# Optimization experiments

Hardware: AMD Instinct MI355X
Metric: run time of the kernel (lower is better)

## Reference

```python
import jax, jax.numpy as jnp
import numpy as np

N, E, F_IN, F_E, HID, HEADS = 20000, 320000, 256, 32, 128, 4
NEG_SLOPE = 0.2  # PyG GATConv default negative_slope


def _segment_softmax(logits, seg, num_segments):
    # logits: [E, H] softmax over edges sharing the same destination node
    m = jax.ops.segment_max(logits, seg, num_segments=num_segments)
    m = jnp.where(jnp.isfinite(m), m, 0.0)
    e = jnp.exp(logits - m[seg])
    s = jax.ops.segment_sum(e, seg, num_segments=num_segments)
    return e / s[seg]


def _gat_layer(x, edge_attr, src, dst, W, We, a_src, a_dst, a_edge, bias, num_nodes):
    H, C = a_src.shape
    h = (x @ W).reshape(-1, H, C)            # [N, H, C]
    he = (edge_attr @ We).reshape(-1, H, C)  # [E, H, C]
    alpha = (h * a_src).sum(-1)[src] + (h * a_dst).sum(-1)[dst] + (he * a_edge).sum(-1)
    alpha = jax.nn.leaky_relu(alpha, NEG_SLOPE)          # [E, H]
    alpha = _segment_softmax(alpha, dst, num_nodes)
    out = jax.ops.segment_sum(h[src] * alpha[..., None], dst, num_segments=num_nodes)
    return out.reshape(num_nodes, H * C) + bias


def setup_inputs() -> dict:
    key = jax.random.key(0)
    ks = jax.random.split(key, 20)
    s1 = 1.0 / np.sqrt(F_IN)
    s2 = 1.0 / np.sqrt(HID * HEADS)
    se = 1.0 / np.sqrt(F_E)
    sh = 1.0 / np.sqrt(HID)
    return {
        "x": jax.random.normal(ks[0], (N, F_IN), jnp.float32),
        "edge_index": jax.random.randint(ks[1], (2, E), 0, N),
        "edge_attr": jax.random.normal(ks[2], (E, F_E), jnp.float32),
        # GAT layer 1: in=F_IN, heads=HEADS, out=HID, concat=True
        "W1": jax.random.normal(ks[3], (F_IN, HEADS * HID), jnp.float32) * s1,
        "We1": jax.random.normal(ks[4], (F_E, HEADS * HID), jnp.float32) * se,
        "as1": jax.random.normal(ks[5], (HEADS, HID), jnp.float32) * sh,
        "ad1": jax.random.normal(ks[6], (HEADS, HID), jnp.float32) * sh,
        "ae1": jax.random.normal(ks[7], (HEADS, HID), jnp.float32) * sh,
        "b1": jnp.zeros((HEADS * HID,), jnp.float32),
        # GAT layer 2: in=HEADS*HID, heads=1, out=HID
        "W2": jax.random.normal(ks[8], (HEADS * HID, HID), jnp.float32) * s2,
        "We2": jax.random.normal(ks[9], (F_E, HID), jnp.float32) * se,
        "as2": jax.random.normal(ks[10], (1, HID), jnp.float32) * sh,
        "ad2": jax.random.normal(ks[11], (1, HID), jnp.float32) * sh,
        "ae2": jax.random.normal(ks[12], (1, HID), jnp.float32) * sh,
        "b2": jnp.zeros((HID,), jnp.float32),
        # projection head: Linear(HID,HID) -> PReLU -> Linear(HID,HID)
        "P1": jax.random.normal(ks[13], (HID, HID), jnp.float32) * sh,
        "pb1": jnp.zeros((HID,), jnp.float32),
        "prelu_a": jnp.float32(0.25),
        "P2": jax.random.normal(ks[14], (HID, HID), jnp.float32) * sh,
        "pb2": jnp.zeros((HID,), jnp.float32),
    }


def reference(x, edge_index, edge_attr, W1, We1, as1, ad1, ae1, b1,
              W2, We2, as2, ad2, ae2, b2, P1, pb1, prelu_a, P2, pb2):
    # eval mode: edge dropout / feature dropout are no-ops
    ei = jnp.concatenate([edge_index, edge_index[::-1]], axis=1)  # add reversed edges
    ea = jnp.concatenate([edge_attr, edge_attr], axis=0)
    src, dst = ei[0], ei[1]
    n = x.shape[0]
    h = jax.nn.elu(_gat_layer(x, ea, src, dst, W1, We1, as1, ad1, ae1, b1, n))
    h = jax.nn.elu(_gat_layer(h, ea, src, dst, W2, We2, as2, ad2, ae2, b2, n))
    z = h @ P1 + pb1
    z = jnp.where(z > 0, z, prelu_a * z)  # PReLU (single shared parameter)
    h_proj = z @ P2 + pb2
    g = jax.nn.sigmoid(h_proj.mean(axis=0))
    return h_proj, g
```

## Files before the change

### kernel.cpp

```cpp
#include <hip/hip_runtime.h>
#include <hip/hip_bf16.h>


#define NN    20000
#define EE    320000
#define E2    640000
#define FIN   256
#define FE    32
#define HIDD  128
#define NHEAD 4
#define HH    512
#define CAP   160
#define AW    132

typedef unsigned short ushort_t;
typedef short frag8 __attribute__((ext_vector_type(8)));
typedef float f32x4 __attribute__((ext_vector_type(4)));

__device__ inline ushort_t f2bf(float f){
  unsigned x = __float_as_uint(f);
  unsigned r = (x + 0x7fffu + ((x>>16)&1u)) >> 16;
  return (ushort_t)r;
}
__device__ inline float bf2f(ushort_t u){ return __uint_as_float(((unsigned)u)<<16); }
__device__ inline float lo_of(unsigned v){ return __uint_as_float(v<<16); }
__device__ inline float hi_of(unsigned v){ return __uint_as_float(v & 0xffff0000u); }

__global__ void prep(const int* __restrict__ ei, int* __restrict__ cnt,
                     const float* __restrict__ x, ushort_t* __restrict__ xb,
                     const float* __restrict__ W1, ushort_t* __restrict__ W1t,
                     const float* __restrict__ W2, ushort_t* __restrict__ W2t,
                     const float* __restrict__ P1, ushort_t* __restrict__ P1th, ushort_t* __restrict__ P1tl,
                     const float* __restrict__ P2, ushort_t* __restrict__ P2th, ushort_t* __restrict__ P2tl,
                     const float* __restrict__ We1, const float* __restrict__ ae1,
                     const float* __restrict__ We2, const float* __restrict__ ae2,
                     float* __restrict__ v1, float* __restrict__ v2){
  int b = blockIdx.x, tid = threadIdx.x;
  if(b < 2500){
    int e = b*256 + tid;
    int dst = (e < EE) ? ei[EE + e] : ei[e - EE];
    atomicAdd(&cnt[dst], 1);
  } else if(b < 7500){
    int i = (b-2500)*256 + tid;
    float4 v = ((const float4*)x)[i];
    ushort4 o; o.x=f2bf(v.x); o.y=f2bf(v.y); o.z=f2bf(v.z); o.w=f2bf(v.w);
    ((ushort4*)xb)[i] = o;
  } else if(b < 8012){
    int idx = (b-7500)*256 + tid;
    int k = idx>>9, n = idx&511;
    W1t[n*FIN + k] = f2bf(W1[idx]);
  } else if(b < 8268){
    int idx = (b-8012)*256 + tid;
    int k = idx>>7, n = idx&127;
    W2t[n*HH + k] = f2bf(W2[idx]);
  } else if(b < 8332){
    int idx = (b-8268)*256 + tid;
    int k = idx>>7, n = idx&127;
    float v = P1[idx];
    ushort_t h = f2bf(v);
    P1th[n*HIDD + k] = h;
    P1tl[n*HIDD + k] = f2bf(v - bf2f(h));
  } else if(b < 8396){
    int idx = (b-8332)*256 + tid;
    int k = idx>>7, n = idx&127;
    float v = P2[idx];
    ushort_t h = f2bf(v);
    P2th[n*HIDD + k] = h;
    P2tl[n*HIDD + k] = f2bf(v - bf2f(h));
  } else {
    if(tid < FE*NHEAD){
      int f = tid>>2, h = tid&3;
      float s = 0.f;
      for(int c=0;c<HIDD;c++) s += We1[f*HH + h*HIDD + c] * ae1[h*HIDD + c];
      v1[f*4+h] = s;
    } else if(tid < FE*NHEAD + FE){
      int f = tid - FE*NHEAD;
      float s = 0.f;
      for(int c=0;c<HIDD;c++) s += We2[f*HIDD + c] * ae2[c];
      v2[f] = s;
    }
  }
}

__global__ void scan_k(const int* __restrict__ cnt, int* __restrict__ rowptr){
  __shared__ int sums[1024];
  int tid = threadIdx.x;
  const int per = 20;
  int base = tid*per;
  int v[20];
  if(base + per <= NN){
    #pragma unroll
    for(int q=0;q<5;q++) *(int4*)&v[q*4] = *(const int4*)&cnt[base + q*4];
  } else {
    for(int i=0;i<per;i++) v[i] = (base+i<NN)? cnt[base+i] : 0;
  }
  int s = 0;
  #pragma unroll
  for(int i=0;i<per;i++) s += v[i];
  sums[tid] = s; __syncthreads();
  for(int off=1; off<1024; off<<=1){
    int t = (tid>=off)? sums[tid-off] : 0;
    __syncthreads();
    sums[tid] += t;
    __syncthreads();
  }
  int run = (tid==0)? 0 : sums[tid-1];
  int rp[20];
  #pragma unroll
  for(int i=0;i<per;i++){ rp[i] = run; run += v[i]; }
  if(base + per <= NN){
    #pragma unroll
    for(int q=0;q<5;q++) *(int4*)&rowptr[base + q*4] = *(const int4*)&rp[q*4];
  } else {
    for(int i=0;i<per;i++) if(base+i<=NN) rowptr[base+i] = rp[i];
  }
  if(tid == 1000) rowptr[NN] = rp[0];
}

__global__ __launch_bounds__(256) void csr_gemm1(
    const int* __restrict__ ei, const float* __restrict__ ea,
    const float* __restrict__ v1, const float* __restrict__ v2,
    const int* __restrict__ rowptr, int* __restrict__ fcnt,
    int* __restrict__ csrc, float* __restrict__ cae1, float* __restrict__ cae2,
    const ushort_t* __restrict__ A, const ushort_t* __restrict__ Bt,
    ushort_t* __restrict__ C, int M,
    const float* __restrict__ as1, const float* __restrict__ ad1,
    float* __restrict__ s1n, float* __restrict__ d1n){
  __shared__ ushort_t As[128*32];
  __shared__ ushort_t Bs[128*32];
  __shared__ float sred[2][128], dred[2][128];
  __shared__ float sv1[FE*NHEAD];
  __shared__ float sv2[FE];
  int tid = threadIdx.x;
  int b = blockIdx.x;
  if(b < 1250){
    if(tid < FE*NHEAD) sv1[tid] = v1[tid];
    if(tid < FE)       sv2[tid] = v2[tid];
    __syncthreads();
    int e = b*256 + tid;
    int a = ei[e], bb = ei[EE+e];
    const float4* er4 = (const float4*)(ea + (long)e*FE);
    float a0=0,a1=0,a2=0,a3=0,ab=0;
    #pragma unroll
    for(int f4=0; f4<FE/4; f4++){
      float4 t = er4[f4];
      float tv[4] = {t.x, t.y, t.z, t.w};
      #pragma unroll
      for(int c=0;c<4;c++){
        int f = f4*4+c;
        float t1 = tv[c];
        a0 += t1*sv1[f*4+0]; a1 += t1*sv1[f*4+1]; a2 += t1*sv1[f*4+2]; a3 += t1*sv1[f*4+3];
        ab += t1*sv2[f];
      }
    }
    float4 c4; c4.x=a0; c4.y=a1; c4.z=a2; c4.w=a3;
    int pos = rowptr[bb] + atomicAdd(&fcnt[bb], 1);
    csrc[pos] = a;
    *(float4*)(cae1 + (size_t)pos*4) = c4;
    cae2[pos] = ab;
    pos = rowptr[a] + atomicAdd(&fcnt[a], 1);
    csrc[pos] = bb;
    *(float4*)(cae1 + (size_t)pos*4) = c4;
    cae2[pos] = ab;
    return;
  }
  int g = b - 1250;
  int head = g & 3;
  int m0 = (g>>2)*128, n0 = head*128;
  int w = tid>>6, lane = tid&63;
  int qr = (w>>1)*64, qc = (w&1)*64;
  int lrow = lane&15, koff = (lane>>4)*8;
  f32x4 acc[4][4] = {};
  for(int k0=0; k0<FIN; k0+=32){
    #pragma unroll
    for(int rep=0;rep<2;rep++){
      int segid = tid + rep*256;
      int row = segid>>2, off = (segid&3)*8;
      int gr = m0 + row;
      int4 va = (gr<M) ? *(const int4*)(A + (long)gr*FIN + k0 + off) : int4{0,0,0,0};
      *(int4*)&As[row*32 + off] = va;
      int4 vb = *(const int4*)(Bt + (long)(n0+row)*FIN + k0 + off);
      *(int4*)&Bs[row*32 + off] = vb;
    }
    __syncthreads();
    frag8 af[4], bfr[4];
    #pragma unroll
    for(int i=0;i<4;i++) af[i]  = *(const frag8*)&As[(qr + i*16 + lrow)*32 + koff];
    #pragma unroll
    for(int j=0;j<4;j++) bfr[j] = *(const frag8*)&Bs[(qc + j*16 + lrow)*32 + koff];
    #pragma unroll
    for(int i=0;i<4;i++)
      #pragma unroll
      for(int j=0;j<4;j++)
        acc[i][j] = __builtin_amdgcn_mfma_f32_16x16x32_bf16(af[i], bfr[j], acc[i][j], 0,0,0);
    __syncthreads();
  }
  #pragma unroll
  for(int i=0;i<4;i++)
    #pragma unroll
    for(int j=0;j<4;j++)
      #pragma unroll
      for(int r=0;r<4;r++){
        int row = m0 + qr + i*16 + (lane>>4)*4 + r;
        int col = n0 + qc + j*16 + (lane&15);
        if(row<M) C[(long)row*HH + col] = f2bf(acc[i][j][r]);
      }
  float a_s[4], a_d[4];
  #pragma unroll
  for(int j=0;j<4;j++){
    a_s[j] = as1[head*HIDD + qc + j*16 + (lane&15)];
    a_d[j] = ad1[head*HIDD + qc + j*16 + (lane&15)];
  }
  #pragma unroll
  for(int i=0;i<4;i++)
    #pragma unroll
    for(int r=0;r<4;r++){
      float sp = acc[i][0][r]*a_s[0] + acc[i][1][r]*a_s[1] + acc[i][2][r]*a_s[2] + acc[i][3][r]*a_s[3];
      float dp = acc[i][0][r]*a_d[0] + acc[i][1][r]*a_d[1] + acc[i][2][r]*a_d[2] + acc[i][3][r]*a_d[3];
      #pragma unroll
      for(int o=1;o<=8;o<<=1){ sp += __shfl_xor(sp,o,64); dp += __shfl_xor(dp,o,64); }
      if((lane&15)==0){
        int rl = qr + i*16 + (lane>>4)*4 + r;
        sred[w&1][rl] = sp;
        dred[w&1][rl] = dp;
      }
    }
  __syncthreads();
  if(tid < 128){
    int gr = m0 + tid;
    if(gr < M){
      s1n[gr*4 + head] = sred[0][tid] + sred[1][tid];
      d1n[gr*4 + head] = dred[0][tid] + dred[1][tid];
    }
  }
}

__global__ __launch_bounds__(256) void gemm64_attn(const ushort_t* __restrict__ A, const ushort_t* __restrict__ Bt,
                                                   ushort_t* __restrict__ C, int M,
                                                   const float* __restrict__ as2, const float* __restrict__ ad2,
                                                   float* __restrict__ s2n, float* __restrict__ d2n){
  __shared__ ushort_t As[64*32];
  __shared__ ushort_t Bs[128*32];
  __shared__ float sred[4][64], dred[4][64];
  int tid = threadIdx.x;
  int m0 = blockIdx.y*64;
  int w = tid>>6, lane = tid&63;
  int qc = w*32;
  int lrow = lane&15, koff = (lane>>4)*8;
  f32x4 acc[4][2] = {};
  for(int k0=0; k0<HH; k0+=32){
    {
      int row = tid>>2, off = (tid&3)*8;
      int gr = m0 + row;
      int4 va = (gr<M) ? *(const int4*)(A + (long)gr*HH + k0 + off) : int4{0,0,0,0};
      *(int4*)&As[row*32 + off] = va;
    }
    #pragma unroll
    for(int rep=0;rep<2;rep++){
      int segid = tid + rep*256;
      int row = segid>>2, off = (segid&3)*8;
      int4 vb = *(const int4*)(Bt + (long)row*HH + k0 + off);
      *(int4*)&Bs[row*32 + off] = vb;
    }
    __syncthreads();
    frag8 af[4], bfr[2];
    #pragma unroll
    for(int i=0;i<4;i++) af[i]  = *(const frag8*)&As[(i*16 + lrow)*32 + koff];
    #pragma unroll
    for(int j=0;j<2;j++) bfr[j] = *(const frag8*)&Bs[(qc + j*16 + lrow)*32 + koff];
    #pragma unroll
    for(int i=0;i<4;i++)
      #pragma unroll
      for(int j=0;j<2;j++)
        acc[i][j] = __builtin_amdgcn_mfma_f32_16x16x32_bf16(af[i], bfr[j], acc[i][j], 0,0,0);
    __syncthreads();
  }
  #pragma unroll
  for(int i=0;i<4;i++)
    #pragma unroll
    for(int j=0;j<2;j++)
      #pragma unroll
      for(int r=0;r<4;r++){
        int row = m0 + i*16 + (lane>>4)*4 + r;
        int col = qc + j*16 + (lane&15);
        if(row<M) C[(long)row*HIDD + col] = f2bf(acc[i][j][r]);
      }
  float a_s[2], a_d[2];
  #pragma unroll
  for(int j=0;j<2;j++){
    a_s[j] = as2[qc + j*16 + (lane&15)];
    a_d[j] = ad2[qc + j*16 + (lane&15)];
  }
  #pragma unroll
  for(int i=0;i<4;i++)
    #pragma unroll
    for(int r=0;r<4;r++){
      float sp = acc[i][0][r]*a_s[0] + acc[i][1][r]*a_s[1];
      float dp = acc[i][0][r]*a_d[0] + acc[i][1][r]*a_d[1];
      #pragma unroll
      for(int o=1;o<=8;o<<=1){ sp += __shfl_xor(sp,o,64); dp += __shfl_xor(dp,o,64); }
      if((lane&15)==0){
        int rl = i*16 + (lane>>4)*4 + r;
        sred[w][rl] = sp;
        dred[w][rl] = dp;
      }
    }
  __syncthreads();
  if(tid < 64){
    int gr = m0 + tid;
    if(gr < M){
      s2n[gr] = sred[0][tid]+sred[1][tid]+sred[2][tid]+sred[3][tid];
      d2n[gr] = dred[0][tid]+dred[1][tid]+dred[2][tid]+dred[3][tid];
    }
  }
}

__global__ __launch_bounds__(256) void agg1(const ushort_t* __restrict__ h1b, const int* __restrict__ rowptr,
                     const int* __restrict__ csrc,
                     const float* __restrict__ s1n, const float* __restrict__ d1n,
                     const float* __restrict__ cae1,
                     const float* __restrict__ b1, ushort_t* __restrict__ out1b){
  __shared__ float stw[2][CAP*4];
  __shared__ int   sidx[2][CAP];
  __shared__ float pm[2][2][4], ps[2][2][4];
  __shared__ float part[2][8][64];
  int tid = threadIdx.x;
  int nodeLoc = tid>>7;
  int wv = (tid>>6)&1;
  int lane = tid&63;
  int n = blockIdx.x*2 + nodeLoc;
  int beg = rowptr[n], end = rowptr[n+1];
  int deg = end - beg;
  int h12 = lane&3;
  float dh = d1n[n*4 + h12];
  float m = -1e30f, ss = 0.f;
  for(int base=beg + wv*16; base<end; base+=32){
    int e = base + (lane>>2);
    if(e<end){
      int s = csrc[e];
      float t = s1n[s*4 + h12] + dh + cae1[e*4 + h12];
      t = t>0.f? t : 0.2f*t;
      int j = e - beg;
      if(j < CAP){
        stw[nodeLoc][j*4 + h12] = t;
        if(h12==0) sidx[nodeLoc][j] = s;
      }
      float nm = fmaxf(m, t);
      ss = ss*__expf(m-nm) + __expf(t-nm);
      m = nm;
    }
  }
  #pragma unroll
  for(int o=4;o<=32;o<<=1){
    float mo = __shfl_xor(m, o, 64), so = __shfl_xor(ss, o, 64);
    float nm = fmaxf(m, mo);
    ss = ss*__expf(m-nm) + so*__expf(mo-nm);
    m = nm;
  }
  if(lane<4){ pm[nodeLoc][wv][lane] = m; ps[nodeLoc][wv][lane] = ss; }
  __syncthreads();
  float m4[4], i4[4];
  #pragma unroll
  for(int h=0;h<4;h++){
    float mA = pm[nodeLoc][0][h], mB = pm[nodeLoc][1][h];
    float sA = ps[nodeLoc][0][h], sB = ps[nodeLoc][1][h];
    float mf = fmaxf(mA, mB);
    float sf = sA*__expf(mA-mf) + sB*__expf(mB-mf);
    m4[h] = mf; i4[h] = sf>0.f ? 1.f/sf : 0.f;
  }
  int capn = deg < CAP ? deg : CAP;
  int tln = tid & 127;
  float mh = m4[h12], ih = i4[h12];
  for(int f=tln; f<capn*4; f+=128) stw[nodeLoc][f] = __expf(stw[nodeLoc][f]-mh)*ih;
  __syncthreads();
  int hq = lane>>4;
  int half = (capn+1)>>1;
  int gb = wv*half;
  int ge = (gb+half < capn) ? gb+half : capn;
  float acc[8] = {};
  int j = gb;
  for(; j+3<ge; j+=4){
    int s0 = sidx[nodeLoc][j],   s1 = sidx[nodeLoc][j+1];
    int s2 = sidx[nodeLoc][j+2], s3 = sidx[nodeLoc][j+3];
    float w0 = stw[nodeLoc][(j  )*4 + hq];
    float w1 = stw[nodeLoc][(j+1)*4 + hq];
    float w2 = stw[nodeLoc][(j+2)*4 + hq];
    float w3 = stw[nodeLoc][(j+3)*4 + hq];
    uint4 v0 = *(const uint4*)(h1b + (long)s0*HH + lane*8);
    uint4 v1 = *(const uint4*)(h1b + (long)s1*HH + lane*8);
    uint4 v2 = *(const uint4*)(h1b + (long)s2*HH + lane*8);
    uint4 v3 = *(const uint4*)(h1b + (long)s3*HH + lane*8);
    acc[0] += w0*lo_of(v0.x) + w1*lo_of(v1.x) + w2*lo_of(v2.x) + w3*lo_of(v3.x);
    acc[1] += w0*hi_of(v0.x) + w1*hi_of(v1.x) + w2*hi_of(v2.x) + w3*hi_of(v3.x);
    acc[2] += w0*lo_of(v0.y) + w1*lo_of(v1.y) + w2*lo_of(v2.y) + w3*lo_of(v3.y);
    acc[3] += w0*hi_of(v0.y) + w1*hi_of(v1.y) + w2*hi_of(v2.y) + w3*hi_of(v3.y);
    acc[4] += w0*lo_of(v0.z) + w1*lo_of(v1.z) + w2*lo_of(v2.z) + w3*lo_of(v3.z);
    acc[5] += w0*hi_of(v0.z) + w1*hi_of(v1.z) + w2*hi_of(v2.z) + w3*hi_of(v3.z);
    acc[6] += w0*lo_of(v0.w) + w1*lo_of(v1.w) + w2*lo_of(v2.w) + w3*lo_of(v3.w);
    acc[7] += w0*hi_of(v0.w) + w1*hi_of(v1.w) + w2*hi_of(v2.w) + w3*hi_of(v3.w);
  }
  for(; j<ge; j++){
    int s0 = sidx[nodeLoc][j];
    float w0 = stw[nodeLoc][j*4 + hq];
    uint4 v0 = *(const uint4*)(h1b + (long)s0*HH + lane*8);
    acc[0] += w0*lo_of(v0.x); acc[1] += w0*hi_of(v0.x);
    acc[2] += w0*lo_of(v0.y); acc[3] += w0*hi_of(v0.y);
    acc[4] += w0*lo_of(v0.z); acc[5] += w0*hi_of(v0.z);
    acc[6] += w0*lo_of(v0.w); acc[7] += w0*hi_of(v0.w);
  }
  for(int jj=CAP+wv; jj<deg; jj+=2){
    int e = beg + jj;
    int s0 = csrc[e];
    float t = s1n[s0*4 + hq] + d1n[n*4 + hq] + cae1[e*4 + hq];
    t = t>0.f? t : 0.2f*t;
    float w0 = __expf(t - m4[hq])*i4[hq];
    uint4 v0 = *(const uint4*)(h1b + (long)s0*HH + lane*8);
    acc[0] += w0*lo_of(v0.x); acc[1] += w0*hi_of(v0.x);
    acc[2] += w0*lo_of(v0.y); acc[3] += w0*hi_of(v0.y);
    acc[4] += w0*lo_of(v0.z); acc[5] += w0*hi_of(v0.z);
    acc[6] += w0*lo_of(v0.w); acc[7] += w0*hi_of(v0.w);
  }
  if(wv==1){
    #pragma unroll
    for(int c=0;c<8;c++) part[nodeLoc][c][lane] = acc[c];
  }
  __syncthreads();
  if(wv==0){
    #pragma unroll
    for(int c=0;c<8;c++) acc[c] += part[nodeLoc][c][lane];
    float4 bl = ((const float4*)b1)[lane*2];
    float4 bh = ((const float4*)b1)[lane*2+1];
    float bb[8] = {bl.x,bl.y,bl.z,bl.w,bh.x,bh.y,bh.z,bh.w};
    ushort_t o8[8];
    #pragma unroll
    for(int c=0;c<8;c++){
      float o = acc[c] + bb[c];
      o8[c] = f2bf(o>0.f? o : __expf(o)-1.f);
    }
    uint4 pk;
    pk.x = (unsigned)o8[0] | ((unsigned)o8[1]<<16);
    pk.y = (unsigned)o8[2] | ((unsigned)o8[3]<<16);
    pk.z = (unsigned)o8[4] | ((unsigned)o8[5]<<16);
    pk.w = (unsigned)o8[6] | ((unsigned)o8[7]<<16);
    *(uint4*)(out1b + (long)n*HH + lane*8) = pk;
  }
}

__global__ __launch_bounds__(256) void agg2(const ushort_t* __restrict__ h2b, const int* __restrict__ rowptr,
                     const int* __restrict__ csrc,
                     const float* __restrict__ s2n, const float* __restrict__ d2n,
                     const float* __restrict__ cae2,
                     const float* __restrict__ b2, float* __restrict__ out2){
  __shared__ float stl[2][CAP];
  __shared__ int   sid[2][CAP];
  __shared__ float pm2[2][2], ps2[2][2];
  __shared__ float part2[2][2][64];
  int tid = threadIdx.x;
  int nodeLoc = tid>>7;
  int wv = (tid>>6)&1;
  int lane = tid&63;
  int n = blockIdx.x*2 + nodeLoc;
  int beg = rowptr[n], end = rowptr[n+1];
  int deg = end - beg;
  float dn = d2n[n];
  float m = -1e30f, ss = 0.f;
  for(int e=beg + wv*64 + lane; e<end; e+=128){
    int s = csrc[e];
    float t = s2n[s] + dn + cae2[e];
    t = t>0.f? t : 0.2f*t;
    int j = e - beg;
    if(j < CAP){ stl[nodeLoc][j] = t; sid[nodeLoc][j] = s; }
    float nm = fmaxf(m, t);
    ss = ss*__expf(m-nm) + __expf(t-nm);
    m = nm;
  }
  #pragma unroll
  for(int o=1;o<=32;o<<=1){
    float mo = __shfl_xor(m, o, 64), so = __shfl_xor(ss, o, 64);
    float nm = fmaxf(m, mo);
    ss = ss*__expf(m-nm) + so*__expf(mo-nm);
    m = nm;
  }
  if(lane==0){ pm2[nodeLoc][wv] = m; ps2[nodeLoc][wv] = ss; }
  __syncthreads();
  {
    float mA = pm2[nodeLoc][0], mB = pm2[nodeLoc][1];
    float sA = ps2[nodeLoc][0], sB = ps2[nodeLoc][1];
    m = fmaxf(mA, mB);
    ss = sA*__expf(mA-m) + sB*__expf(mB-m);
  }
  float inv = ss>0.f ? 1.f/ss : 0.f;
  int capn = deg < CAP ? deg : CAP;
  for(int j=tid&127; j<capn; j+=128) stl[nodeLoc][j] = __expf(stl[nodeLoc][j]-m)*inv;
  __syncthreads();
  int half = (capn+1)>>1;
  int gb = wv*half;
  int ge = (gb+half < capn) ? gb+half : capn;
  float a0=0.f, a1=0.f;
  int j = gb;
  for(; j+3<ge; j+=4){
    int s0 = sid[nodeLoc][j], s1 = sid[nodeLoc][j+1], s2 = sid[nodeLoc][j+2], s3 = sid[nodeLoc][j+3];
    float w0 = stl[nodeLoc][j], w1 = stl[nodeLoc][j+1], w2 = stl[nodeLoc][j+2], w3 = stl[nodeLoc][j+3];
    unsigned v0 = *(const unsigned*)(h2b + (long)s0*HIDD + 2*lane);
    unsigned v1 = *(const unsigned*)(h2b + (long)s1*HIDD + 2*lane);
    unsigned v2 = *(const unsigned*)(h2b + (long)s2*HIDD + 2*lane);
    unsigned v3 = *(const unsigned*)(h2b + (long)s3*HIDD + 2*lane);
    a0 += w0*lo_of(v0) + w1*lo_of(v1) + w2*lo_of(v2) + w3*lo_of(v3);
    a1 += w0*hi_of(v0) + w1*hi_of(v1) + w2*hi_of(v2) + w3*hi_of(v3);
  }
  for(; j<ge; j++){
    float w0 = stl[nodeLoc][j];
    unsigned v0 = *(const unsigned*)(h2b + (long)sid[nodeLoc][j]*HIDD + 2*lane);
    a0 += w0*lo_of(v0); a1 += w0*hi_of(v0);
  }
  for(int jj=CAP+wv; jj<deg; jj+=2){
    int e = beg + jj;
    int s0 = csrc[e];
    float t = s2n[s0] + dn + cae2[e];
    t = t>0.f? t : 0.2f*t;
    float w0 = __expf(t-m)*inv;
    unsigned v0 = *(const unsigned*)(h2b + (long)s0*HIDD + 2*lane);
    a0 += w0*lo_of(v0); a1 += w0*hi_of(v0);
  }
  if(wv==1){
    part2[nodeLoc][0][lane] = a0;
    part2[nodeLoc][1][lane] = a1;
  }
  __syncthreads();
  if(wv==0){
    a0 += part2[nodeLoc][0][lane];
    a1 += part2[nodeLoc][1][lane];
    float o0 = a0 + b2[2*lane];
    float o1 = a1 + b2[2*lane+1];
    float2 pk;
    pk.x = o0>0.f? o0 : __expf(o0)-1.f;
    pk.y = o1>0.f? o1 : __expf(o1)-1.f;
    *(float2*)(out2 + (long)n*HIDD + 2*lane) = pk;
  }
}

__global__ __launch_bounds__(256) void proj_fused(const float* __restrict__ A,
    const ushort_t* __restrict__ P1th, const ushort_t* __restrict__ P1tl,
    const ushort_t* __restrict__ P2th, const ushort_t* __restrict__ P2tl,
    const float* __restrict__ pb1, const float* __restrict__ pra,
    const float* __restrict__ pb2, float* __restrict__ OUT, int M,
    float* __restrict__ gbuf){
  __shared__ ushort_t Ah[64*AW], Al[64*AW];
  __shared__ ushort_t Bh[128*32], Bl[128*32];
  int tid = threadIdx.x;
  int m0 = blockIdx.x*64;
  int w = tid>>6, lane = tid&63;
  int qc = w*32;
  int lrow = lane&15, koff2 = (lane>>4)*8;
  f32x4 acc[4][2] = {};
  {
    int row = tid>>2, cb = (tid&3)*8;
    int gr = m0 + row;
    for(int c0=0;c0<HIDD;c0+=32){
      float4 u0{0,0,0,0}, u1{0,0,0,0};
      if(gr<M){
        u0 = *(const float4*)(A + (long)gr*HIDD + c0 + cb);
        u1 = *(const float4*)(A + (long)gr*HIDD + c0 + cb + 4);
      }
      float vv[8] = {u0.x,u0.y,u0.z,u0.w,u1.x,u1.y,u1.z,u1.w};
      unsigned ph[4], pl[4];
      #pragma unroll
      for(int c=0;c<4;c++){
        ushort_t h0 = f2bf(vv[2*c]),   l0 = f2bf(vv[2*c]   - bf2f(h0));
        ushort_t h1 = f2bf(vv[2*c+1]), l1 = f2bf(vv[2*c+1] - bf2f(h1));
        ph[c] = (unsigned)h0 | ((unsigned)h1<<16);
        pl[c] = (unsigned)l0 | ((unsigned)l1<<16);
      }
      *(uint4*)&Ah[row*AW + c0 + cb] = *(uint4*)ph;
      *(uint4*)&Al[row*AW + c0 + cb] = *(uint4*)pl;
    }
  }
  __syncthreads();
  for(int k0=0;k0<HIDD;k0+=32){
    #pragma unroll
    for(int rep=0;rep<2;rep++){
      int segid = tid + rep*256;
      int row = segid>>2, off = (segid&3)*8;
      *(int4*)&Bh[row*32 + off] = *(const int4*)(P1th + (long)row*HIDD + k0 + off);
      *(int4*)&Bl[row*32 + off] = *(const int4*)(P1tl + (long)row*HIDD + k0 + off);
    }
    __syncthreads();
    frag8 afh[4], afl[4], bfh[2], bfl[2];
    #pragma unroll
    for(int i=0;i<4;i++){
      afh[i] = *(const frag8*)&Ah[(i*16 + lrow)*AW + k0 + koff2];
      afl[i] = *(const frag8*)&Al[(i*16 + lrow)*AW + k0 + koff2];
    }
    #pragma unroll
    for(int j=0;j<2;j++){
      bfh[j] = *(const frag8*)&Bh[(qc + j*16 + lrow)*32 + koff2];
      bfl[j] = *(const frag8*)&Bl[(qc + j*16 + lrow)*32 + koff2];
    }
    #pragma unroll
    for(int i=0;i<4;i++)
      #pragma unroll
      for(int j=0;j<2;j++){
        acc[i][j] = __builtin_amdgcn_mfma_f32_16x16x32_bf16(afh[i], bfh[j], acc[i][j], 0,0,0);
        acc[i][j] = __builtin_amdgcn_mfma_f32_16x16x32_bf16(afh[i], bfl[j], acc[i][j], 0,0,0);
        acc[i][j] = __builtin_amdgcn_mfma_f32_16x16x32_bf16(afl[i], bfh[j], acc[i][j], 0,0,0);
      }
    __syncthreads();
  }
  float ap = pra[0];
  #pragma unroll
  for(int i=0;i<4;i++)
    #pragma unroll
    for(int j=0;j<2;j++)
      #pragma unroll
      for(int r=0;r<4;r++){
        int row = i*16 + (lane>>4)*4 + r;
        int col = qc + j*16 + (lane&15);
        float v = acc[i][j][r] + pb1[col];
        v = v>0.f? v : ap*v;
        ushort_t h = f2bf(v);
        Ah[row*AW + col] = h;
        Al[row*AW + col] = f2bf(v - bf2f(h));
        acc[i][j][r] = 0.f;
      }
  __syncthreads();
  for(int k0=0;k0<HIDD;k0+=32){
    #pragma unroll
    for(int rep=0;rep<2;rep++){
      int segid = tid + rep*256;
      int row = segid>>2, off = (segid&3)*8;
      *(int4*)&Bh[row*32 + off] = *(const int4*)(P2th + (long)row*HIDD + k0 + off);
      *(int4*)&Bl[row*32 + off] = *(const int4*)(P2tl + (long)row*HIDD + k0 + off);
    }
    __syncthreads();
    frag8 afh[4], afl[4], bfh[2], bfl[2];
    #pragma unroll
    for(int i=0;i<4;i++){
      afh[i] = *(const frag8*)&Ah[(i*16 + lrow)*AW + k0 + koff2];
      afl[i] = *(const frag8*)&Al[(i*16 + lrow)*AW + k0 + koff2];
    }
    #pragma unroll
    for(int j=0;j<2;j++){
      bfh[j] = *(const frag8*)&Bh[(qc + j*16 + lrow)*32 + koff2];
      bfl[j] = *(const frag8*)&Bl[(qc + j*16 + lrow)*32 + koff2];
    }
    #pragma unroll
    for(int i=0;i<4;i++)
      #pragma unroll
      for(int j=0;j<2;j++){
        acc[i][j] = __builtin_amdgcn_mfma_f32_16x16x32_bf16(afh[i], bfh[j], acc[i][j], 0,0,0);
        acc[i][j] = __builtin_amdgcn_mfma_f32_16x16x32_bf16(afh[i], bfl[j], acc[i][j], 0,0,0);
        acc[i][j] = __builtin_amdgcn_mfma_f32_16x16x32_bf16(afl[i], bfh[j], acc[i][j], 0,0,0);
      }
    __syncthreads();
  }
  float cs[2] = {0.f, 0.f};
  #pragma unroll
  for(int i=0;i<4;i++)
    #pragma unroll
    for(int j=0;j<2;j++)
      #pragma unroll
      for(int r=0;r<4;r++){
        int rowg = m0 + i*16 + (lane>>4)*4 + r;
        int col = qc + j*16 + (lane&15);
        if(rowg<M){
          float v = acc[i][j][r] + pb2[col];
          OUT[(long)rowg*HIDD + col] = v;
          cs[j] += v;
        }
      }
  #pragma unroll
  for(int j=0;j<2;j++){
    cs[j] += __shfl_xor(cs[j],16,64);
    cs[j] += __shfl_xor(cs[j],32,64);
    if((lane>>4)==0) atomicAdd(&gbuf[qc + j*16 + (lane&15)], cs[j]);
  }
}

__global__ void sigmoid_g(const float* __restrict__ gbuf, float* __restrict__ gout){
  int c = threadIdx.x;
  float m = gbuf[c] * (1.0f/NN);
  gout[c] = 1.f/(1.f+__expf(-m));
}


extern "C" void kernel_launch(void* const* d_in, const int* in_sizes, int n_in,
                              void* d_out, int out_size, void* d_ws, size_t ws_size,
                              hipStream_t stream){
  const float* x    = (const float*)d_in[0];
  const int*   ei   = (const int*)  d_in[1];
  const float* ea   = (const float*)d_in[2];
  const float* W1   = (const float*)d_in[3];
  const float* We1  = (const float*)d_in[4];
  const float* as1  = (const float*)d_in[5];
  const float* ad1  = (const float*)d_in[6];
  const float* ae1  = (const float*)d_in[7];
  const float* b1   = (const float*)d_in[8];
  const float* W2   = (const float*)d_in[9];
  const float* We2  = (const float*)d_in[10];
  const float* as2  = (const float*)d_in[11];
  const float* ad2  = (const float*)d_in[12];
  const float* ae2  = (const float*)d_in[13];
  const float* b2   = (const float*)d_in[14];
  const float* P1   = (const float*)d_in[15];
  const float* pb1  = (const float*)d_in[16];
  const float* pra  = (const float*)d_in[17];
  const float* P2   = (const float*)d_in[18];
  const float* pb2  = (const float*)d_in[19];
  float* out = (float*)d_out;

  char* wsp = (char*)d_ws;
  size_t off = 0;
  auto alloc = [&](size_t bytes)->char*{
    char* p = wsp + off;
    off += (bytes + 255) & ~(size_t)255;
    return p;
  };
  ushort_t* h1b  = (ushort_t*)alloc(sizeof(ushort_t)*(size_t)NN*HH);
  ushort_t* out1b= (ushort_t*)alloc(sizeof(ushort_t)*(size_t)NN*HH);
  ushort_t* h2b  = (ushort_t*)alloc(sizeof(ushort_t)*(size_t)NN*HIDD);
  float*    out2 = (float*)  alloc(sizeof(float)*(size_t)NN*HIDD);
  ushort_t* xb   = (ushort_t*)alloc(sizeof(ushort_t)*(size_t)NN*FIN);
  ushort_t* W1t  = (ushort_t*)alloc(sizeof(ushort_t)*(size_t)HH*FIN);
  ushort_t* W2t  = (ushort_t*)alloc(sizeof(ushort_t)*(size_t)HIDD*HH);
  ushort_t* P1th = (ushort_t*)alloc(sizeof(ushort_t)*(size_t)HIDD*HIDD);
  ushort_t* P1tl = (ushort_t*)alloc(sizeof(ushort_t)*(size_t)HIDD*HIDD);
  ushort_t* P2th = (ushort_t*)alloc(sizeof(ushort_t)*(size_t)HIDD*HIDD);
  ushort_t* P2tl = (ushort_t*)alloc(sizeof(ushort_t)*(size_t)HIDD*HIDD);
  float* s1n   = (float*)alloc(sizeof(float)*NN*NHEAD);
  float* d1n   = (float*)alloc(sizeof(float)*NN*NHEAD);
  float* s2n   = (float*)alloc(sizeof(float)*NN);
  float* d2n   = (float*)alloc(sizeof(float)*NN);
  float* v1    = (float*)alloc(sizeof(float)*FE*NHEAD);
  float* v2    = (float*)alloc(sizeof(float)*FE);
  float* cae1  = (float*)alloc(sizeof(float)*(size_t)E2*NHEAD);
  float* cae2  = (float*)alloc(sizeof(float)*(size_t)E2);
  int*   rowptr= (int*)  alloc(sizeof(int)*(NN+1));
  int*   csrc  = (int*)  alloc(sizeof(int)*(size_t)E2);
  int*   cnt   = (int*)  alloc(sizeof(int)*NN);
  int*   fcnt  = (int*)  alloc(sizeof(int)*NN);
  float* gbuf  = (float*)alloc(sizeof(float)*HIDD);

  hipMemsetAsync(cnt, 0, 80128 + 80128 + 512, stream);

  prep     <<<8397, 256, 0, stream>>>(ei, cnt, x, xb, W1, W1t, W2, W2t,
                                      P1, P1th, P1tl, P2, P2th, P2tl,
                                      We1, ae1, We2, ae2, v1, v2);
  scan_k   <<<1, 1024, 0, stream>>>(cnt, rowptr);
  csr_gemm1<<<1250 + 628, 256, 0, stream>>>(ei, ea, v1, v2, rowptr, fcnt, csrc, cae1, cae2,
                                            xb, W1t, h1b, NN, as1, ad1, s1n, d1n);
  agg1     <<<NN/2, 256, 0, stream>>>(h1b, rowptr, csrc, s1n, d1n, cae1, b1, out1b);
  gemm64_attn<<<dim3(1, (NN+63)/64), 256, 0, stream>>>(out1b, W2t, h2b, NN, as2, ad2, s2n, d2n);
  agg2     <<<NN/2, 256, 0, stream>>>(h2b, rowptr, csrc, s2n, d2n, cae2, b2, out2);
  proj_fused<<<(NN+63)/64, 256, 0, stream>>>(out2, P1th, P1tl, P2th, P2tl,
                                             pb1, pra, pb2, out, NN, gbuf);
  sigmoid_g<<<1, 128, 0, stream>>>(gbuf, out + (size_t)NN*HIDD);
}
```

Measured before the change: 381.4 us.

## Store edge ids in CSR slots, split edge and GEMM kernels, one-wave agg2

The CSR build now writes (neighbor, original edge id) pairs, and per-edge attention terms are written once per original edge rather than scattered twice into CSR order. This cuts scattered float4 writes and halves the cae buffers. The cost is an extra indirection in the aggregation kernels. The fused edge/GEMM kernel is split into two separate launches. agg2 now handles four nodes per block with one wave per node, which removes block syncs and the cross-wave reduction.

Result: slower. 389.2 us (+2.0%).

```diff
diff --git a/kernel.cpp b/kernel.cpp
--- a/kernel.cpp
+++ b/kernel.cpp
@@ -117,28 +117,26 @@
   if(tid == 1000) rowptr[NN] = rp[0];
 }
 
-__global__ __launch_bounds__(256) void csr_gemm1(
-    const int* __restrict__ ei, const float* __restrict__ ea,
-    const float* __restrict__ v1, const float* __restrict__ v2,
-    const int* __restrict__ rowptr, int* __restrict__ fcnt,
-    int* __restrict__ csrc, float* __restrict__ cae1, float* __restrict__ cae2,
-    const ushort_t* __restrict__ A, const ushort_t* __restrict__ Bt,
-    ushort_t* __restrict__ C, int M,
-    const float* __restrict__ as1, const float* __restrict__ ad1,
-    float* __restrict__ s1n, float* __restrict__ d1n){
-  __shared__ ushort_t As[128*32];
-  __shared__ ushort_t Bs[128*32];
-  __shared__ float sred[2][128], dred[2][128];
-  __shared__ float sv1[FE*NHEAD];
-  __shared__ float sv2[FE];
-  int tid = threadIdx.x;
-  int b = blockIdx.x;
+__global__ void csr_edge(const int* __restrict__ ei, const float* __restrict__ ea,
+                         const float* __restrict__ v1, const float* __restrict__ v2,
+                         const int* __restrict__ rowptr, int* __restrict__ fcnt,
+                         int2* __restrict__ eslot,
+                         float* __restrict__ cae1, float* __restrict__ cae2){
+  int b = blockIdx.x, tid = threadIdx.x;
   if(b < 1250){
+    int e = b*256 + tid;
+    int a = ei[e], bb = ei[EE+e];
+    int p1 = rowptr[bb] + atomicAdd(&fcnt[bb], 1);
+    int p2 = rowptr[a]  + atomicAdd(&fcnt[a],  1);
+    eslot[p1] = make_int2(a,  e);
+    eslot[p2] = make_int2(bb, e);
+  } else {
+    __shared__ float sv1[FE*NHEAD];
+    __shared__ float sv2[FE];
     if(tid < FE*NHEAD) sv1[tid] = v1[tid];
     if(tid < FE)       sv2[tid] = v2[tid];
     __syncthreads();
-    int e = b*256 + tid;
-    int a = ei[e], bb = ei[EE+e];
+    int e = (b-1250)*256 + tid;
     const float4* er4 = (const float4*)(ea + (long)e*FE);
     float a0=0,a1=0,a2=0,a3=0,ab=0;
     #pragma unroll
@@ -154,19 +152,21 @@
       }
     }
     float4 c4; c4.x=a0; c4.y=a1; c4.z=a2; c4.w=a3;
-    int pos = rowptr[bb] + atomicAdd(&fcnt[bb], 1);
-    csrc[pos] = a;
-    *(float4*)(cae1 + (size_t)pos*4) = c4;
-    cae2[pos] = ab;
-    pos = rowptr[a] + atomicAdd(&fcnt[a], 1);
-    csrc[pos] = bb;
-    *(float4*)(cae1 + (size_t)pos*4) = c4;
-    cae2[pos] = ab;
-    return;
-  }
-  int g = b - 1250;
-  int head = g & 3;
-  int m0 = (g>>2)*128, n0 = head*128;
+    *(float4*)(cae1 + (size_t)e*4) = c4;
+    cae2[e] = ab;
+  }
+}
+
+__global__ __launch_bounds__(256) void gemm1_attn(const ushort_t* __restrict__ A, const ushort_t* __restrict__ Bt,
+                                                  ushort_t* __restrict__ C, int M,
+                                                  const float* __restrict__ as1, const float* __restrict__ ad1,
+                                                  float* __restrict__ s1n, float* __restrict__ d1n){
+  __shared__ ushort_t As[128*32];
+  __shared__ ushort_t Bs[128*32];
+  __shared__ float sred[2][128], dred[2][128];
+  int tid = threadIdx.x;
+  int head = blockIdx.x;
+  int m0 = blockIdx.y*128, n0 = head*128;
   int w = tid>>6, lane = tid&63;
   int qr = (w>>1)*64, qc = (w&1)*64;
   int lrow = lane&15, koff = (lane>>4)*8;
@@ -316,7 +316,7 @@
 }
 
 __global__ __launch_bounds__(256) void agg1(const ushort_t* __restrict__ h1b, const int* __restrict__ rowptr,
-                     const int* __restrict__ csrc,
+                     const int2* __restrict__ eslot,
                      const float* __restrict__ s1n, const float* __restrict__ d1n,
                      const float* __restrict__ cae1,
                      const float* __restrict__ b1, ushort_t* __restrict__ out1b){
@@ -337,13 +337,13 @@
   for(int base=beg + wv*16; base<end; base+=32){
     int e = base + (lane>>2);
     if(e<end){
-      int s = csrc[e];
-      float t = s1n[s*4 + h12] + dh + cae1[e*4 + h12];
+      int2 se = eslot[e];
+      float t = s1n[se.x*4 + h12] + dh + cae1[(size_t)se.y*4 + h12];
       t = t>0.f? t : 0.2f*t;
       int j = e - beg;
       if(j < CAP){
         stw[nodeLoc][j*4 + h12] = t;
-        if(h12==0) sidx[nodeLoc][j] = s;
+        if(h12==0) sidx[nodeLoc][j] = se.x;
       }
       float nm = fmaxf(m, t);
       ss = ss*__expf(m-nm) + __expf(t-nm);
@@ -410,11 +410,11 @@
   }
   for(int jj=CAP+wv; jj<deg; jj+=2){
     int e = beg + jj;
-    int s0 = csrc[e];
-    float t = s1n[s0*4 + hq] + d1n[n*4 + hq] + cae1[e*4 + hq];
+    int2 se = eslot[e];
+    float t = s1n[se.x*4 + hq] + d1n[n*4 + hq] + cae1[(size_t)se.y*4 + hq];
     t = t>0.f? t : 0.2f*t;
     float w0 = __expf(t - m4[hq])*i4[hq];
-    uint4 v0 = *(const uint4*)(h1b + (long)s0*HH + lane*8);
+    uint4 v0 = *(const uint4*)(h1b + (long)se.x*HH + lane*8);
     acc[0] += w0*lo_of(v0.x); acc[1] += w0*hi_of(v0.x);
     acc[2] += w0*lo_of(v0.y); acc[3] += w0*hi_of(v0.y);
     acc[4] += w0*lo_of(v0.z); acc[5] += w0*hi_of(v0.z);
@@ -447,29 +447,25 @@
 }
 
 __global__ __launch_bounds__(256) void agg2(const ushort_t* __restrict__ h2b, const int* __restrict__ rowptr,
-                     const int* __restrict__ csrc,
+                     const int2* __restrict__ eslot,
                      const float* __restrict__ s2n, const float* __restrict__ d2n,
                      const float* __restrict__ cae2,
                      const float* __restrict__ b2, float* __restrict__ out2){
-  __shared__ float stl[2][CAP];
-  __shared__ int   sid[2][CAP];
-  __shared__ float pm2[2][2], ps2[2][2];
-  __shared__ float part2[2][2][64];
+  __shared__ float stl[4][CAP];
+  __shared__ int   sid[4][CAP];
   int tid = threadIdx.x;
-  int nodeLoc = tid>>7;
-  int wv = (tid>>6)&1;
-  int lane = tid&63;
-  int n = blockIdx.x*2 + nodeLoc;
+  int wv = tid>>6, lane = tid&63;
+  int n = blockIdx.x*4 + wv;
   int beg = rowptr[n], end = rowptr[n+1];
   int deg = end - beg;
   float dn = d2n[n];
   float m = -1e30f, ss = 0.f;
-  for(int e=beg + wv*64 + lane; e<end; e+=128){
-    int s = csrc[e];
-    float t = s2n[s] + dn + cae2[e];
+  for(int e=beg+lane; e<end; e+=64){
+    int2 se = eslot[e];
+    float t = s2n[se.x] + dn + cae2[se.y];
     t = t>0.f? t : 0.2f*t;
     int j = e - beg;
-    if(j < CAP){ stl[nodeLoc][j] = t; sid[nodeLoc][j] = s; }
+    if(j < CAP){ stl[wv][j] = t; sid[wv][j] = se.x; }
     float nm = fmaxf(m, t);
     ss = ss*__expf(m-nm) + __expf(t-nm);
     m = nm;
@@ -481,26 +477,14 @@
     ss = ss*__expf(m-nm) + so*__expf(mo-nm);
     m = nm;
   }
-  if(lane==0){ pm2[nodeLoc][wv] = m; ps2[nodeLoc][wv] = ss; }
-  __syncthreads();
-  {
-    float mA = pm2[nodeLoc][0], mB = pm2[nodeLoc][1];
-    float sA = ps2[nodeLoc][0], sB = ps2[nodeLoc][1];
-    m = fmaxf(mA, mB);
-    ss = sA*__expf(mA-m) + sB*__expf(mB-m);
-  }
   float inv = ss>0.f ? 1.f/ss : 0.f;
   int capn = deg < CAP ? deg : CAP;
-  for(int j=tid&127; j<capn; j+=128) stl[nodeLoc][j] = __expf(stl[nodeLoc][j]-m)*inv;
-  __syncthreads();
-  int half = (capn+1)>>1;
-  int gb = wv*half;
-  int ge = (gb+half < capn) ? gb+half : capn;
+  for(int j=lane; j<capn; j+=64) stl[wv][j] = __expf(stl[wv][j]-m)*inv;
   float a0=0.f, a1=0.f;
-  int j = gb;
-  for(; j+3<ge; j+=4){
-    int s0 = sid[nodeLoc][j], s1 = sid[nodeLoc][j+1], s2 = sid[nodeLoc][j+2], s3 = sid[nodeLoc][j+3];
-    float w0 = stl[nodeLoc][j], w1 = stl[nodeLoc][j+1], w2 = stl[nodeLoc][j+2], w3 = stl[nodeLoc][j+3];
+  int j = 0;
+  for(; j+3<capn; j+=4){
+    int s0 = sid[wv][j], s1 = sid[wv][j+1], s2 = sid[wv][j+2], s3 = sid[wv][j+3];
+    float w0 = stl[wv][j], w1 = stl[wv][j+1], w2 = stl[wv][j+2], w3 = stl[wv][j+3];
     unsigned v0 = *(const unsigned*)(h2b + (long)s0*HIDD + 2*lane);
     unsigned v1 = *(const unsigned*)(h2b + (long)s1*HIDD + 2*lane);
     unsigned v2 = *(const unsigned*)(h2b + (long)s2*HIDD + 2*lane);
@@ -508,35 +492,26 @@
     a0 += w0*lo_of(v0) + w1*lo_of(v1) + w2*lo_of(v2) + w3*lo_of(v3);
     a1 += w0*hi_of(v0) + w1*hi_of(v1) + w2*hi_of(v2) + w3*hi_of(v3);
   }
-  for(; j<ge; j++){
-    float w0 = stl[nodeLoc][j];
-    unsigned v0 = *(const unsigned*)(h2b + (long)sid[nodeLoc][j]*HIDD + 2*lane);
+  for(; j<capn; j++){
+    float w0 = stl[wv][j];
+    unsigned v0 = *(const unsigned*)(h2b + (long)sid[wv][j]*HIDD + 2*lane);
     a0 += w0*lo_of(v0); a1 += w0*hi_of(v0);
   }
-  for(int jj=CAP+wv; jj<deg; jj+=2){
-    int e = beg + jj;
-    int s0 = csrc[e];
-    float t = s2n[s0] + dn + cae2[e];
+  for(; j<deg; j++){
+    int e = beg + j;
+    int2 se = eslot[e];
+    float t = s2n[se.x] + dn + cae2[se.y];
     t = t>0.f? t : 0.2f*t;
     float w0 = __expf(t-m)*inv;
-    unsigned v0 = *(const unsigned*)(h2b + (long)s0*HIDD + 2*lane);
+    unsigned v0 = *(const unsigned*)(h2b + (long)se.x*HIDD + 2*lane);
     a0 += w0*lo_of(v0); a1 += w0*hi_of(v0);
   }
-  if(wv==1){
-    part2[nodeLoc][0][lane] = a0;
-    part2[nodeLoc][1][lane] = a1;
-  }
-  __syncthreads();
-  if(wv==0){
-    a0 += part2[nodeLoc][0][lane];
-    a1 += part2[nodeLoc][1][lane];
-    float o0 = a0 + b2[2*lane];
-    float o1 = a1 + b2[2*lane+1];
-    float2 pk;
-    pk.x = o0>0.f? o0 : __expf(o0)-1.f;
-    pk.y = o1>0.f? o1 : __expf(o1)-1.f;
-    *(float2*)(out2 + (long)n*HIDD + 2*lane) = pk;
-  }
+  float o0 = a0 + b2[2*lane];
+  float o1 = a1 + b2[2*lane+1];
+  float2 pk;
+  pk.x = o0>0.f? o0 : __expf(o0)-1.f;
+  pk.y = o1>0.f? o1 : __expf(o1)-1.f;
+  *(float2*)(out2 + (long)n*HIDD + 2*lane) = pk;
 }
 
 __global__ __launch_bounds__(256) void proj_fused(const float* __restrict__ A,
@@ -732,10 +707,10 @@
   float* d2n   = (float*)alloc(sizeof(float)*NN);
   float* v1    = (float*)alloc(sizeof(float)*FE*NHEAD);
   float* v2    = (float*)alloc(sizeof(float)*FE);
-  float* cae1  = (float*)alloc(sizeof(float)*(size_t)E2*NHEAD);
-  float* cae2  = (float*)alloc(sizeof(float)*(size_t)E2);
+  float* cae1  = (float*)alloc(sizeof(float)*(size_t)EE*NHEAD);
+  float* cae2  = (float*)alloc(sizeof(float)*(size_t)EE);
+  int2*  eslot = (int2*) alloc(sizeof(int2)*(size_t)E2);
   int*   rowptr= (int*)  alloc(sizeof(int)*(NN+1));
-  int*   csrc  = (int*)  alloc(sizeof(int)*(size_t)E2);
   int*   cnt   = (int*)  alloc(sizeof(int)*NN);
   int*   fcnt  = (int*)  alloc(sizeof(int)*NN);
   float* gbuf  = (float*)alloc(sizeof(float)*HIDD);
@@ -746,11 +721,11 @@
                                       P1, P1th, P1tl, P2, P2th, P2tl,
                                       We1, ae1, We2, ae2, v1, v2);
   scan_k   <<<1, 1024, 0, stream>>>(cnt, rowptr);
-  csr_gemm1<<<1250 + 628, 256, 0, stream>>>(ei, ea, v1, v2, rowptr, fcnt, csrc, cae1, cae2,
-                                            xb, W1t, h1b, NN, as1, ad1, s1n, d1n);
-  agg1     <<<NN/2, 256, 0, stream>>>(h1b, rowptr, csrc, s1n, d1n, cae1, b1, out1b);
+  csr_edge <<<2500, 256, 0, stream>>>(ei, ea, v1, v2, rowptr, fcnt, eslot, cae1, cae2);
+  gemm1_attn<<<dim3(NHEAD, (NN+127)/128), 256, 0, stream>>>(xb, W1t, h1b, NN, as1, ad1, s1n, d1n);
+  agg1     <<<NN/2, 256, 0, stream>>>(h1b, rowptr, eslot, s1n, d1n, cae1, b1, out1b);
   gemm64_attn<<<dim3(1, (NN+63)/64), 256, 0, stream>>>(out1b, W2t, h2b, NN, as2, ad2, s2n, d2n);
-  agg2     <<<NN/2, 256, 0, stream>>>(h2b, rowptr, csrc, s2n, d2n, cae2, b2, out2);
+  agg2     <<<NN/4, 256, 0, stream>>>(h2b, rowptr, eslot, s2n, d2n, cae2, b2, out2);
   proj_fused<<<(NN+63)/64, 256, 0, stream>>>(out2, P1th, P1tl, P2th, P2tl,
                                              pb1, pra, pb2, out, NN, gbuf);
   sigmoid_g<<<1, 128, 0, stream>>>(gbuf, out + (size_t)NN*HIDD);
```
